# Kernel optimization log

Measured on AMD Instinct MI355X. Metric: run time of the kernel, lower is better.

## Reference

```python
import jax, jax.numpy as jnp
import numpy as np

DIM = 768
HEADS = 12
MLP_DIM = 3072
EPS = 1e-5


def setup_inputs() -> dict:
    key = jax.random.key(0)
    ks = jax.random.split(key, 10)
    s = lambda d: 1.0 / np.sqrt(d)
    return {
        "x": jax.random.normal(ks[0], (8, 1024, DIM), dtype=jnp.float32),
        "ln1_g": jnp.ones((DIM,), jnp.float32),
        "ln1_b": jnp.zeros((DIM,), jnp.float32),
        "w_qkv": jax.random.normal(ks[1], (DIM, 3 * DIM), jnp.float32) * s(DIM),
        "w_out": jax.random.normal(ks[2], (DIM, DIM), jnp.float32) * s(DIM),
        "b_out": jnp.zeros((DIM,), jnp.float32),
        "ln2_g": jnp.ones((DIM,), jnp.float32),
        "ln2_b": jnp.zeros((DIM,), jnp.float32),
        "w1": jax.random.normal(ks[3], (DIM, MLP_DIM), jnp.float32) * s(DIM),
        "b1": jnp.zeros((MLP_DIM,), jnp.float32),
        "w2": jax.random.normal(ks[4], (MLP_DIM, DIM), jnp.float32) * s(MLP_DIM),
        "b2": jnp.zeros((DIM,), jnp.float32),
    }


def _layernorm(x, g, b):
    mu = jnp.mean(x, axis=-1, keepdims=True)
    var = jnp.mean(jnp.square(x - mu), axis=-1, keepdims=True)
    return (x - mu) * jax.lax.rsqrt(var + EPS) * g + b


def _block(x, ln1_g, ln1_b, w_qkv, w_out, b_out, ln2_g, ln2_b, w1, b1, w2, b2):
    B, N, C = x.shape
    H = HEADS
    Dh = C // H
    scale = Dh ** -0.5
    # attention
    h = _layernorm(x, ln1_g, ln1_b)
    qkv = (h @ w_qkv).reshape(B, N, 3, H, Dh)
    q, k, v = qkv[:, :, 0], qkv[:, :, 1], qkv[:, :, 2]  # [B,N,H,Dh]
    attn = jnp.einsum("bnhd,bmhd->bhnm", q, k) * scale
    attn = jax.nn.softmax(attn, axis=-1)
    o = jnp.einsum("bhnm,bmhd->bnhd", attn, v).reshape(B, N, C)
    x = x + o @ w_out + b_out
    # mlp (exact erf GELU, matching torch nn.GELU default)
    h = _layernorm(x, ln2_g, ln2_b)
    h = jax.nn.gelu(h @ w1 + b1, approximate=False)
    x = x + h @ w2 + b2
    return x


def reference(x, ln1_g, ln1_b, w_qkv, w_out, b_out, ln2_g, ln2_b, w1, b1, w2, b2):
    return _block(x, ln1_g, ln1_b, w_qkv, w_out, b_out, ln2_g, ln2_b, w1, b1, w2, b2)
```

## Files before the change

### kernel.cpp

```cpp
#include <hip/hip_runtime.h>
#include <hip/hip_bf16.h>
#include <cstdint>

#define DIM 768
#define HEADS 12
#define DH 64
#define MLP_DIM 3072
#define ROWS 8192
#define SEQ 1024
#define PPAD 72

typedef __attribute__((ext_vector_type(8))) short bf16x8;
typedef __attribute__((ext_vector_type(4))) float f32x4;

typedef __attribute__((address_space(1))) void GV;
typedef __attribute__((address_space(3))) void SV;

__device__ inline void async16(const void* g, void* l) {
  __builtin_amdgcn_global_load_lds((GV*)(void*)g, (SV*)l, 16, 0, 0);
}

__device__ inline unsigned short f2b(float f) {
  union { float f; uint32_t u; } v; v.f = f;
  uint32_t u = v.u;
  return (unsigned short)((u + 0x7fffu + ((u >> 16) & 1u)) >> 16);
}

__device__ inline float gelu_f(float v) {
  float x = v * 0.70710678118654752f;
  float ax = fabsf(x);
  float t = 1.f / (1.f + 0.47047f * ax);
  float poly = t * (0.3480242f + t * (-0.0958798f + t * 0.7478556f));
  float erfv = 1.f - poly * __expf(-ax * ax);
  erfv = copysignf(erfv, x);
  return 0.5f * v * (1.f + erfv);
}

__global__ __launch_bounds__(256) void transpose_k(const float* __restrict__ in,
                                                   unsigned short* __restrict__ out,
                                                   int K, int N) {
  __shared__ float t[32][33];
  int tx = threadIdx.x & 31, ty = threadIdx.x >> 5;
  int bn = blockIdx.x * 32, bk = blockIdx.y * 32;
#pragma unroll
  for (int i = ty; i < 32; i += 8) t[i][tx] = in[(size_t)(bk + i) * N + bn + tx];
  __syncthreads();
#pragma unroll
  for (int i = ty; i < 32; i += 8) out[(size_t)(bn + i) * K + bk + tx] = f2b(t[tx][i]);
}

__global__ __launch_bounds__(256) void ln_k(const float* __restrict__ x,
                                            const float* __restrict__ g,
                                            const float* __restrict__ b,
                                            unsigned short* __restrict__ h) {
  int wave = threadIdx.x >> 6, lane = threadIdx.x & 63;
  int row = blockIdx.x * 4 + wave;
  const float* xr = x + (size_t)row * DIM;
  float v[12];
  float s = 0.f;
#pragma unroll
  for (int j = 0; j < 12; ++j) { v[j] = xr[lane + j * 64]; s += v[j]; }
#pragma unroll
  for (int m = 1; m < 64; m <<= 1) s += __shfl_xor(s, m);
  float mu = s * (1.f / DIM);
  float vs = 0.f;
#pragma unroll
  for (int j = 0; j < 12; ++j) { float d = v[j] - mu; vs += d * d; }
#pragma unroll
  for (int m = 1; m < 64; m <<= 1) vs += __shfl_xor(vs, m);
  float rstd = rsqrtf(vs * (1.f / DIM) + 1e-5f);
  unsigned short* hr = h + (size_t)row * DIM;
#pragma unroll
  for (int j = 0; j < 12; ++j) {
    int i = lane + j * 64;
    hr[i] = f2b((v[j] - mu) * rstd * g[i] + b[i]);
  }
}

template <int MODE, int TM>
__global__ __launch_bounds__(256, 2) void gemm_k(
    const unsigned short* __restrict__ A, const unsigned short* __restrict__ Bt,
    int M, int N, int K,
    const float* __restrict__ bias, const float* __restrict__ resid,
    float* __restrict__ outf, unsigned short* __restrict__ outb,
    unsigned short* __restrict__ Qb, unsigned short* __restrict__ Kb,
    unsigned short* __restrict__ Vt) {
  constexpr int MI = (TM == 128) ? 4 : 2;
  __shared__ __align__(16) unsigned short As[TM * 64];
  __shared__ __align__(16) unsigned short Bs[128 * 64];
  int tid = threadIdx.x;
  int wave = tid >> 6, lane = tid & 63, lrow = lane & 15, qd = lane >> 4;
  int ntn = N >> 7;
  int bm = (blockIdx.x / ntn) * TM;
  int bn = (blockIdx.x % ntn) << 7;
  int wm = (TM == 128) ? (wave >> 1) * 64 : (wave & 1) * 32;
  int wn = (TM == 128) ? (wave & 1) * 64 : (wave >> 1) * 64;

  f32x4 acc[MI][4];
#pragma unroll
  for (int i = 0; i < MI; ++i)
#pragma unroll
    for (int j = 0; j < 4; ++j) acc[i][j] = (f32x4){0.f, 0.f, 0.f, 0.f};

  int srow = tid >> 3;
  int c = (tid & 7) ^ (srow & 7);
  const char* gA = (const char*)(A + (size_t)(bm + srow) * K) + c * 16;
  const char* gB = (const char*)(Bt + (size_t)(bn + srow) * K) + c * 16;
  char* lA = (char*)As + tid * 16;
  char* lB = (char*)Bs + tid * 16;
  size_t rstep = (size_t)32 * K * 2;

  int nk = K >> 6;
  for (int kt = 0; kt < nk; ++kt) {
    size_t ko = (size_t)kt * 128;
#pragma unroll
    for (int j = 0; j < TM / 32; ++j) async16(gA + ko + j * rstep, lA + j * 4096);
#pragma unroll
    for (int j = 0; j < 4; ++j) async16(gB + ko + j * rstep, lB + j * 4096);
    asm volatile("s_waitcnt vmcnt(0)" ::: "memory");
    __syncthreads();
#pragma unroll
    for (int s = 0; s < 2; ++s) {
      int q = s * 4 + qd;
      bf16x8 af[MI], bfr[4];
#pragma unroll
      for (int i = 0; i < MI; ++i) {
        int r = wm + i * 16 + lrow;
        af[i] = *(const bf16x8*)(As + r * 64 + ((q ^ (r & 7)) << 3));
      }
#pragma unroll
      for (int i = 0; i < 4; ++i) {
        int r = wn + i * 16 + lrow;
        bfr[i] = *(const bf16x8*)(Bs + r * 64 + ((q ^ (r & 7)) << 3));
      }
#pragma unroll
      for (int mi = 0; mi < MI; ++mi)
#pragma unroll
        for (int ni = 0; ni < 4; ++ni)
          acc[mi][ni] = __builtin_amdgcn_mfma_f32_16x16x32_bf16(af[mi], bfr[ni], acc[mi][ni], 0, 0, 0);
    }
    __syncthreads();
  }

#pragma unroll
  for (int mi = 0; mi < MI; ++mi)
#pragma unroll
    for (int ni = 0; ni < 4; ++ni)
#pragma unroll
      for (int r = 0; r < 4; ++r) {
        int row = bm + wm + mi * 16 + qd * 4 + r;
        int col = bn + wn + ni * 16 + lrow;
        float v = acc[mi][ni][r];
        if (MODE == 0) {
          int which = col / 768;
          int rem = col - which * 768;
          int hh = rem >> 6, dh = rem & 63;
          int bb = row >> 10, n = row & 1023;
          size_t bh = (size_t)(bb * HEADS + hh);
          if (which == 0) {
            Qb[(bh * SEQ + n) * DH + dh] = f2b(v * 0.125f);
          } else if (which == 1) {
            Kb[(bh * SEQ + n) * DH + (((dh >> 3) ^ (n & 7)) << 3) + (dh & 7)] = f2b(v);
          } else {
            Vt[(bh * DH + dh) * SEQ + (n & ~63) +
               ((((n >> 3) & 7) ^ (dh & 7)) << 3) + (n & 7)] = f2b(v);
          }
        } else if (MODE == 1) {
          v += bias[col] + resid[(size_t)row * 768 + col];
          outf[(size_t)row * 768 + col] = v;
        } else {
          v += bias[col];
          outb[(size_t)row * MLP_DIM + col] = f2b(gelu_f(v));
        }
      }
}

__global__ __launch_bounds__(256, 3) void attn_k(const unsigned short* __restrict__ Qb,
                                                 const unsigned short* __restrict__ Kb,
                                                 const unsigned short* __restrict__ Vt,
                                                 unsigned short* __restrict__ o) {
  __shared__ __align__(16) unsigned short Ks[2][64 * 64];
  __shared__ __align__(16) unsigned short Vs[2][64 * 64];
  __shared__ __align__(16) unsigned short Pa[4][32 * PPAD];
  int tid = threadIdx.x;
  int wave = tid >> 6, lane = tid & 63;
  int lrow = lane & 15, qd = lane >> 4;
  int bh = blockIdx.x % 96;
  int qt = blockIdx.x / 96;
  int b = bh / HEADS, hh = bh % HEADS;
  const unsigned short* Qh = Qb + (size_t)bh * SEQ * DH;
  const char* Kh = (const char*)(Kb + (size_t)bh * SEQ * DH);
  const char* Vh = (const char*)(Vt + (size_t)bh * DH * SEQ);
  int qw = qt * 128 + wave * 32;

  bf16x8 qf[2][2];
#pragma unroll
  for (int qs = 0; qs < 2; ++qs)
#pragma unroll
    for (int hf = 0; hf < 2; ++hf)
      qf[qs][hf] = *(const bf16x8*)(Qh + (qw + qs * 16 + lrow) * DH + hf * 32 + qd * 8);

  f32x4 oacc[2][4];
#pragma unroll
  for (int qs = 0; qs < 2; ++qs)
#pragma unroll
    for (int d = 0; d < 4; ++d) oacc[qs][d] = (f32x4){0.f, 0.f, 0.f, 0.f};
  float li[2] = {0.f, 0.f};
  unsigned short* Pw = Pa[wave];

  auto stage = [&](int t, int buf) {
    const char* kbase = Kh + (size_t)t * 8192;
    char* kd = (char*)Ks[buf];
    async16(kbase + tid * 16, kd + tid * 16);
    async16(kbase + 4096 + tid * 16, kd + 4096 + tid * 16);
    const char* vbase = Vh + (size_t)t * 128;
    char* vd = (char*)Vs[buf];
    async16(vbase + (size_t)(tid >> 3) * 2048 + (tid & 7) * 16, vd + tid * 16);
    async16(vbase + (size_t)((tid >> 3) + 32) * 2048 + (tid & 7) * 16, vd + 4096 + tid * 16);
  };

  stage(0, 0);
  for (int t = 0; t < 16; ++t) {
    asm volatile("s_waitcnt vmcnt(0)" ::: "memory");
    __syncthreads();
    if (t < 15) stage(t + 1, (t + 1) & 1);
    const unsigned short* Kst = Ks[t & 1];
    const unsigned short* Vst = Vs[t & 1];

    f32x4 st[4][2];
#pragma unroll
    for (int kt = 0; kt < 4; ++kt) {
      int krow = kt * 16 + lrow;
      int ksw = krow & 7;
      const unsigned short* Kr = Kst + krow * 64;
      bf16x8 k0 = *(const bf16x8*)(Kr + ((qd ^ ksw) << 3));
      bf16x8 k1 = *(const bf16x8*)(Kr + (((qd + 4) ^ ksw) << 3));
#pragma unroll
      for (int qs = 0; qs < 2; ++qs) {
        f32x4 z = (f32x4){0.f, 0.f, 0.f, 0.f};
        z = __builtin_amdgcn_mfma_f32_16x16x32_bf16(k0, qf[qs][0], z, 0, 0, 0);
        z = __builtin_amdgcn_mfma_f32_16x16x32_bf16(k1, qf[qs][1], z, 0, 0, 0);
        st[kt][qs] = z;
      }
    }

#pragma unroll
    for (int kt = 0; kt < 4; ++kt)
#pragma unroll
      for (int qs = 0; qs < 2; ++qs) {
        float p0 = __expf(st[kt][qs][0]);
        float p1 = __expf(st[kt][qs][1]);
        float p2 = __expf(st[kt][qs][2]);
        float p3 = __expf(st[kt][qs][3]);
        li[qs] += (p0 + p1) + (p2 + p3);
        uint2 pk;
        pk.x = (uint32_t)f2b(p0) | ((uint32_t)f2b(p1) << 16);
        pk.y = (uint32_t)f2b(p2) | ((uint32_t)f2b(p3) << 16);
        *(uint2*)(Pw + (qs * 16 + lrow) * PPAD + kt * 16 + qd * 4) = pk;
      }
    asm volatile("s_waitcnt lgkmcnt(0)" ::: "memory");

    bf16x8 ap[2][2];
#pragma unroll
    for (int qs = 0; qs < 2; ++qs)
#pragma unroll
      for (int kh = 0; kh < 2; ++kh)
        ap[qs][kh] = *(const bf16x8*)(Pw + (qs * 16 + lrow) * PPAD + kh * 32 + qd * 8);

#pragma unroll
    for (int ds = 0; ds < 4; ++ds) {
      int vrow = ds * 16 + lrow;
      int vsw = vrow & 7;
      const unsigned short* Vr = Vst + vrow * 64;
      bf16x8 v0 = *(const bf16x8*)(Vr + ((qd ^ vsw) << 3));
      bf16x8 v1 = *(const bf16x8*)(Vr + (((4 + qd) ^ vsw) << 3));
#pragma unroll
      for (int qs = 0; qs < 2; ++qs) {
        oacc[qs][ds] = __builtin_amdgcn_mfma_f32_16x16x32_bf16(ap[qs][0], v0, oacc[qs][ds], 0, 0, 0);
        oacc[qs][ds] = __builtin_amdgcn_mfma_f32_16x16x32_bf16(ap[qs][1], v1, oacc[qs][ds], 0, 0, 0);
      }
    }
  }

#pragma unroll
  for (int qs = 0; qs < 2; ++qs) {
    li[qs] += __shfl_xor(li[qs], 16);
    li[qs] += __shfl_xor(li[qs], 32);
  }

#pragma unroll
  for (int qs = 0; qs < 2; ++qs)
#pragma unroll
    for (int r = 0; r < 4; ++r) {
      float inv = 1.f / __shfl(li[qs], qd * 4 + r);
      int n = qw + qs * 16 + qd * 4 + r;
#pragma unroll
      for (int ds = 0; ds < 4; ++ds) {
        int dh = ds * 16 + lrow;
        o[((size_t)(b * SEQ + n)) * DIM + hh * DH + dh] = f2b(oacc[qs][ds][r] * inv);
      }
    }
}

extern "C" void kernel_launch(void* const* d_in, const int* in_sizes, int n_in,
                              void* d_out, int out_size, void* d_ws, size_t ws_size,
                              hipStream_t stream) {
  const float* x     = (const float*)d_in[0];
  const float* ln1_g = (const float*)d_in[1];
  const float* ln1_b = (const float*)d_in[2];
  const float* w_qkv = (const float*)d_in[3];
  const float* w_out = (const float*)d_in[4];
  const float* b_out = (const float*)d_in[5];
  const float* ln2_g = (const float*)d_in[6];
  const float* ln2_b = (const float*)d_in[7];
  const float* w1    = (const float*)d_in[8];
  const float* b1    = (const float*)d_in[9];
  const float* w2    = (const float*)d_in[10];
  const float* b2    = (const float*)d_in[11];

  char* ws = (char*)d_ws;
  unsigned short* wqkvT = (unsigned short*)(ws + 0);
  unsigned short* woutT = (unsigned short*)(ws + 3538944);
  unsigned short* w1T   = (unsigned short*)(ws + 4718592);
  unsigned short* w2T   = (unsigned short*)(ws + 9437184);
  float*          x2    = (float*)(ws + 14155776);
  unsigned short* h     = (unsigned short*)(ws + 39321600);
  char* big = ws + 51904512;
  unsigned short* Qb = (unsigned short*)(big);
  unsigned short* Kb = (unsigned short*)(big + 12582912);
  unsigned short* Vt = (unsigned short*)(big + 25165824);
  unsigned short* ob = (unsigned short*)(big + 37748736);
  unsigned short* am = (unsigned short*)(big);

  transpose_k<<<dim3(72, 24), 256, 0, stream>>>(w_qkv, wqkvT, 768, 2304);
  transpose_k<<<dim3(24, 24), 256, 0, stream>>>(w_out, woutT, 768, 768);
  transpose_k<<<dim3(96, 24), 256, 0, stream>>>(w1, w1T, 768, 3072);
  transpose_k<<<dim3(24, 96), 256, 0, stream>>>(w2, w2T, 3072, 768);

  ln_k<<<2048, 256, 0, stream>>>(x, ln1_g, ln1_b, h);
  gemm_k<0, 128><<<64 * 18, 256, 0, stream>>>(h, wqkvT, ROWS, 2304, 768,
                                              nullptr, nullptr, nullptr, nullptr, Qb, Kb, Vt);
  attn_k<<<768, 256, 0, stream>>>(Qb, Kb, Vt, ob);
  gemm_k<1, 64><<<128 * 6, 256, 0, stream>>>(ob, woutT, ROWS, 768, 768,
                                             b_out, x, x2, nullptr, nullptr, nullptr, nullptr);
  ln_k<<<2048, 256, 0, stream>>>(x2, ln2_g, ln2_b, h);
  gemm_k<2, 128><<<64 * 24, 256, 0, stream>>>(h, w1T, ROWS, 3072, 768,
                                              b1, nullptr, nullptr, am, nullptr, nullptr, nullptr);
  gemm_k<1, 64><<<128 * 6, 256, 0, stream>>>(am, w2T, ROWS, 768, 3072,
                                             b2, x2, (float*)d_out, nullptr, nullptr, nullptr, nullptr);
}
```

Before: 357.1 us.

## Double-buffer GEMM K-loop and stage epilogue through LDS for coalesced stores

The GEMM main loop now uses two LDS buffers, so the async global-to-LDS load of the next K tile is issued while MFMAs run on the current tile, and one barrier per iteration is removed. The epilogue is also rewritten: each mode first writes the accumulator tile into shared memory, then issues 16-byte vector stores for Q/K/V (keeping the swizzled layouts), the residual-add output, and the GELU output, replacing scattered 2-byte and 4-byte stores. The cost is doubled LDS use per block, which may reduce occupancy, plus extra barriers and LDS traffic in the epilogue.

After: 391.4 us. +9.6%, slower.

```diff
diff --git a/kernel.cpp b/kernel.cpp
--- a/kernel.cpp
+++ b/kernel.cpp
@@ -9,6 +9,8 @@
 #define ROWS 8192
 #define SEQ 1024
 #define PPAD 72
+#define ISTR 136
+#define FSTR 132
 
 typedef __attribute__((ext_vector_type(8))) short bf16x8;
 typedef __attribute__((ext_vector_type(4))) float f32x4;
@@ -86,8 +88,8 @@
     unsigned short* __restrict__ Qb, unsigned short* __restrict__ Kb,
     unsigned short* __restrict__ Vt) {
   constexpr int MI = (TM == 128) ? 4 : 2;
-  __shared__ __align__(16) unsigned short As[TM * 64];
-  __shared__ __align__(16) unsigned short Bs[128 * 64];
+  constexpr int ASZ = TM * 64, BSZ = 128 * 64;
+  __shared__ __align__(16) unsigned short smem[2 * (ASZ + BSZ)];
   int tid = threadIdx.x;
   int wave = tid >> 6, lane = tid & 63, lrow = lane & 15, qd = lane >> 4;
   int ntn = N >> 7;
@@ -106,19 +108,26 @@
   int c = (tid & 7) ^ (srow & 7);
   const char* gA = (const char*)(A + (size_t)(bm + srow) * K) + c * 16;
   const char* gB = (const char*)(Bt + (size_t)(bn + srow) * K) + c * 16;
-  char* lA = (char*)As + tid * 16;
-  char* lB = (char*)Bs + tid * 16;
   size_t rstep = (size_t)32 * K * 2;
 
+  auto stage = [&](int kt, int buf) {
+    size_t ko = (size_t)kt * 128;
+    char* lA = (char*)(smem + (size_t)buf * (ASZ + BSZ)) + tid * 16;
+    char* lB = lA + ASZ * 2;
+#pragma unroll
+    for (int j = 0; j < TM / 32; ++j) async16(gA + ko + j * rstep, lA + j * 4096);
+#pragma unroll
+    for (int j = 0; j < 4; ++j) async16(gB + ko + j * rstep, lB + j * 4096);
+  };
+
   int nk = K >> 6;
+  stage(0, 0);
   for (int kt = 0; kt < nk; ++kt) {
-    size_t ko = (size_t)kt * 128;
-#pragma unroll
-    for (int j = 0; j < TM / 32; ++j) async16(gA + ko + j * rstep, lA + j * 4096);
-#pragma unroll
-    for (int j = 0; j < 4; ++j) async16(gB + ko + j * rstep, lB + j * 4096);
     asm volatile("s_waitcnt vmcnt(0)" ::: "memory");
     __syncthreads();
+    if (kt + 1 < nk) stage(kt + 1, (kt + 1) & 1);
+    const unsigned short* As = smem + (size_t)(kt & 1) * (ASZ + BSZ);
+    const unsigned short* Bs = As + ASZ;
 #pragma unroll
     for (int s = 0; s < 2; ++s) {
       int q = s * 4 + qd;
@@ -139,40 +148,108 @@
         for (int ni = 0; ni < 4; ++ni)
           acc[mi][ni] = __builtin_amdgcn_mfma_f32_16x16x32_bf16(af[mi], bfr[ni], acc[mi][ni], 0, 0, 0);
     }
+  }
+  __syncthreads();
+
+  if (MODE == 1) {
+    float* img = (float*)smem;
+#pragma unroll
+    for (int mi = 0; mi < MI; ++mi)
+#pragma unroll
+      for (int ni = 0; ni < 4; ++ni)
+#pragma unroll
+        for (int r = 0; r < 4; ++r)
+          img[(wm + mi * 16 + qd * 4 + r) * FSTR + wn + ni * 16 + lrow] = acc[mi][ni][r];
     __syncthreads();
+    int lr = tid >> 2, cs = (tid & 3) * 32;
+    const float* src = img + lr * FSTR + cs;
+    float* dst = outf + (size_t)(bm + lr) * 768 + bn + cs;
+    const float* bp = bias + bn + cs;
+    const float* rp = resid + (size_t)(bm + lr) * 768 + bn + cs;
+#pragma unroll
+    for (int k = 0; k < 8; ++k) {
+      f32x4 v = *(const f32x4*)(src + k * 4);
+      f32x4 bb = *(const f32x4*)(bp + k * 4);
+      f32x4 rr = *(const f32x4*)(rp + k * 4);
+      *(f32x4*)(dst + k * 4) = v + bb + rr;
+    }
+  } else if (MODE == 2) {
+    unsigned short* img = smem;
+#pragma unroll
+    for (int mi = 0; mi < MI; ++mi)
+#pragma unroll
+      for (int ni = 0; ni < 4; ++ni)
+#pragma unroll
+        for (int r = 0; r < 4; ++r) {
+          int lc = wn + ni * 16 + lrow;
+          float v = acc[mi][ni][r] + bias[bn + lc];
+          img[(wm + mi * 16 + qd * 4 + r) * ISTR + lc] = f2b(gelu_f(v));
+        }
+    __syncthreads();
+#pragma unroll
+    for (int p = 0; p < 2; ++p) {
+      int lr = p * 64 + (tid >> 2);
+      int cs = (tid & 3) * 32;
+      const unsigned short* src = img + lr * ISTR + cs;
+      unsigned short* dst = outb + (size_t)(bm + lr) * MLP_DIM + bn + cs;
+#pragma unroll
+      for (int k = 0; k < 4; ++k) *(uint4*)(dst + k * 8) = *(const uint4*)(src + k * 8);
+    }
+  } else {
+    int which = bn / 768;
+    int rem_base = bn - which * 768;
+    unsigned short* img = smem;
+    if (which < 2) {
+#pragma unroll
+      for (int mi = 0; mi < MI; ++mi)
+#pragma unroll
+        for (int ni = 0; ni < 4; ++ni)
+#pragma unroll
+          for (int r = 0; r < 4; ++r) {
+            float v = acc[mi][ni][r];
+            if (which == 0) v *= 0.125f;
+            img[(wm + mi * 16 + qd * 4 + r) * ISTR + wn + ni * 16 + lrow] = f2b(v);
+          }
+      __syncthreads();
+      int lr = tid >> 1, hseg = tid & 1;
+      int hh = rem_base / 64 + hseg;
+      int b = (bm + lr) >> 10, n = (bm + lr) & 1023;
+      size_t bh = (size_t)(b * HEADS + hh);
+      const unsigned short* src = img + lr * ISTR + hseg * 64;
+      unsigned short* dst = (which == 0 ? Qb : Kb) + (bh * SEQ + n) * DH;
+      if (which == 0) {
+#pragma unroll
+        for (int j = 0; j < 8; ++j) *(uint4*)(dst + j * 8) = *(const uint4*)(src + j * 8);
+      } else {
+        int nx = n & 7;
+#pragma unroll
+        for (int j = 0; j < 8; ++j) *(uint4*)(dst + ((j ^ nx) * 8)) = *(const uint4*)(src + j * 8);
+      }
+    } else {
+#pragma unroll
+      for (int mi = 0; mi < MI; ++mi)
+#pragma unroll
+        for (int ni = 0; ni < 4; ++ni) {
+          int lc = wn + ni * 16 + lrow;
+          int rbase = wm + mi * 16 + qd * 4;
+          uint2 pk;
+          pk.x = (uint32_t)f2b(acc[mi][ni][0]) | ((uint32_t)f2b(acc[mi][ni][1]) << 16);
+          pk.y = (uint32_t)f2b(acc[mi][ni][2]) | ((uint32_t)f2b(acc[mi][ni][3]) << 16);
+          *(uint2*)(img + lc * ISTR + rbase) = pk;
+        }
+      __syncthreads();
+      int d = tid >> 1, nh = tid & 1;
+      int hh = rem_base / 64 + (d >> 6);
+      int dhl = d & 63;
+      int b = bm >> 10;
+      size_t bh = (size_t)(b * HEADS + hh);
+      const unsigned short* src = img + d * ISTR + nh * 64;
+      unsigned short* dst = Vt + (bh * DH + dhl) * SEQ + (bm & 1023) + nh * 64;
+      int dx = dhl & 7;
+#pragma unroll
+      for (int j = 0; j < 8; ++j) *(uint4*)(dst + ((j ^ dx) * 8)) = *(const uint4*)(src + j * 8);
+    }
   }
-
-#pragma unroll
-  for (int mi = 0; mi < MI; ++mi)
-#pragma unroll
-    for (int ni = 0; ni < 4; ++ni)
-#pragma unroll
-      for (int r = 0; r < 4; ++r) {
-        int row = bm + wm + mi * 16 + qd * 4 + r;
-        int col = bn + wn + ni * 16 + lrow;
-        float v = acc[mi][ni][r];
-        if (MODE == 0) {
-          int which = col / 768;
-          int rem = col - which * 768;
-          int hh = rem >> 6, dh = rem & 63;
-          int bb = row >> 10, n = row & 1023;
-          size_t bh = (size_t)(bb * HEADS + hh);
-          if (which == 0) {
-            Qb[(bh * SEQ + n) * DH + dh] = f2b(v * 0.125f);
-          } else if (which == 1) {
-            Kb[(bh * SEQ + n) * DH + (((dh >> 3) ^ (n & 7)) << 3) + (dh & 7)] = f2b(v);
-          } else {
-            Vt[(bh * DH + dh) * SEQ + (n & ~63) +
-               ((((n >> 3) & 7) ^ (dh & 7)) << 3) + (n & 7)] = f2b(v);
-          }
-        } else if (MODE == 1) {
-          v += bias[col] + resid[(size_t)row * 768 + col];
-          outf[(size_t)row * 768 + col] = v;
-        } else {
-          v += bias[col];
-          outb[(size_t)row * MLP_DIM + col] = f2b(gelu_f(v));
-        }
-      }
 }
 
 __global__ __launch_bounds__(256, 3) void attn_k(const unsigned short* __restrict__ Qb,
```

## Register-prefetch next GEMM k-tile and stage GELU output through LDS

Applied to the files above, without the earlier changes.

Replaces the async global-to-LDS loads plus full vmcnt wait with register prefetch. The next k-tile is loaded into registers while MFMAs run on the current tile held in LDS. For the MLP-up GEMM, the bf16 GELU results are written to a padded LDS image and then stored to global memory as coalesced 16-byte vectors, instead of scattered 2-byte stores. This costs more registers, which at launch bounds of 2 may cause spills, and adds an extra barrier in the epilogue.

Result: no change. 363.3 us (+1.7%).

```diff
diff --git a/kernel.cpp b/kernel.cpp
--- a/kernel.cpp
+++ b/kernel.cpp
@@ -9,6 +9,7 @@
 #define ROWS 8192
 #define SEQ 1024
 #define PPAD 72
+#define ISTR 136
 
 typedef __attribute__((ext_vector_type(8))) short bf16x8;
 typedef __attribute__((ext_vector_type(4))) float f32x4;
@@ -80,14 +81,15 @@
 template <int MODE, int TM>
 __global__ __launch_bounds__(256, 2) void gemm_k(
     const unsigned short* __restrict__ A, const unsigned short* __restrict__ Bt,
-    int M, int N, int K,
+    int N, int K,
     const float* __restrict__ bias, const float* __restrict__ resid,
     float* __restrict__ outf, unsigned short* __restrict__ outb,
     unsigned short* __restrict__ Qb, unsigned short* __restrict__ Kb,
     unsigned short* __restrict__ Vt) {
   constexpr int MI = (TM == 128) ? 4 : 2;
-  __shared__ __align__(16) unsigned short As[TM * 64];
-  __shared__ __align__(16) unsigned short Bs[128 * 64];
+  constexpr int ASH = TM * 64;
+  constexpr int SMEMS = (TM == 128) ? ((MODE == 2) ? 128 * ISTR : 16384) : 12288;
+  __shared__ __align__(16) unsigned short smem[SMEMS];
   int tid = threadIdx.x;
   int wave = tid >> 6, lane = tid & 63, lrow = lane & 15, qd = lane >> 4;
   int ntn = N >> 7;
@@ -106,19 +108,51 @@
   int c = (tid & 7) ^ (srow & 7);
   const char* gA = (const char*)(A + (size_t)(bm + srow) * K) + c * 16;
   const char* gB = (const char*)(Bt + (size_t)(bn + srow) * K) + c * 16;
-  char* lA = (char*)As + tid * 16;
-  char* lB = (char*)Bs + tid * 16;
+  char* lA = (char*)smem + tid * 16;
+  char* lB = (char*)smem + ASH * 2 + tid * 16;
   size_t rstep = (size_t)32 * K * 2;
+
+  const unsigned short* As = smem;
+  const unsigned short* Bs = smem + ASH;
+
+  uint4 pa0, pa1, pa2, pa3, pb0, pb1, pb2, pb3;
+  pa0 = *(const uint4*)(gA);
+  pa1 = *(const uint4*)(gA + rstep);
+  if constexpr (TM == 128) {
+    pa2 = *(const uint4*)(gA + 2 * rstep);
+    pa3 = *(const uint4*)(gA + 3 * rstep);
+  }
+  pb0 = *(const uint4*)(gB);
+  pb1 = *(const uint4*)(gB + rstep);
+  pb2 = *(const uint4*)(gB + 2 * rstep);
+  pb3 = *(const uint4*)(gB + 3 * rstep);
 
   int nk = K >> 6;
   for (int kt = 0; kt < nk; ++kt) {
-    size_t ko = (size_t)kt * 128;
-#pragma unroll
-    for (int j = 0; j < TM / 32; ++j) async16(gA + ko + j * rstep, lA + j * 4096);
-#pragma unroll
-    for (int j = 0; j < 4; ++j) async16(gB + ko + j * rstep, lB + j * 4096);
-    asm volatile("s_waitcnt vmcnt(0)" ::: "memory");
+    *(uint4*)(lA) = pa0;
+    *(uint4*)(lA + 4096) = pa1;
+    if constexpr (TM == 128) {
+      *(uint4*)(lA + 8192) = pa2;
+      *(uint4*)(lA + 12288) = pa3;
+    }
+    *(uint4*)(lB) = pb0;
+    *(uint4*)(lB + 4096) = pb1;
+    *(uint4*)(lB + 8192) = pb2;
+    *(uint4*)(lB + 12288) = pb3;
     __syncthreads();
+    if (kt + 1 < nk) {
+      size_t k2 = (size_t)(kt + 1) * 128;
+      pa0 = *(const uint4*)(gA + k2);
+      pa1 = *(const uint4*)(gA + k2 + rstep);
+      if constexpr (TM == 128) {
+        pa2 = *(const uint4*)(gA + k2 + 2 * rstep);
+        pa3 = *(const uint4*)(gA + k2 + 3 * rstep);
+      }
+      pb0 = *(const uint4*)(gB + k2);
+      pb1 = *(const uint4*)(gB + k2 + rstep);
+      pb2 = *(const uint4*)(gB + k2 + 2 * rstep);
+      pb3 = *(const uint4*)(gB + k2 + 3 * rstep);
+    }
 #pragma unroll
     for (int s = 0; s < 2; ++s) {
       int q = s * 4 + qd;
@@ -142,16 +176,50 @@
     __syncthreads();
   }
 
-#pragma unroll
-  for (int mi = 0; mi < MI; ++mi)
-#pragma unroll
-    for (int ni = 0; ni < 4; ++ni)
-#pragma unroll
-      for (int r = 0; r < 4; ++r) {
-        int row = bm + wm + mi * 16 + qd * 4 + r;
-        int col = bn + wn + ni * 16 + lrow;
-        float v = acc[mi][ni][r];
-        if (MODE == 0) {
+  if (MODE == 1) {
+#pragma unroll
+    for (int mi = 0; mi < MI; ++mi)
+#pragma unroll
+      for (int ni = 0; ni < 4; ++ni)
+#pragma unroll
+        for (int r = 0; r < 4; ++r) {
+          int row = bm + wm + mi * 16 + qd * 4 + r;
+          int col = bn + wn + ni * 16 + lrow;
+          float v = acc[mi][ni][r] + bias[col] + resid[(size_t)row * 768 + col];
+          outf[(size_t)row * 768 + col] = v;
+        }
+  } else if (MODE == 2) {
+    unsigned short* img = smem;
+#pragma unroll
+    for (int mi = 0; mi < MI; ++mi)
+#pragma unroll
+      for (int ni = 0; ni < 4; ++ni)
+#pragma unroll
+        for (int r = 0; r < 4; ++r) {
+          int lc = wn + ni * 16 + lrow;
+          float v = acc[mi][ni][r] + bias[bn + lc];
+          img[(wm + mi * 16 + qd * 4 + r) * ISTR + lc] = f2b(gelu_f(v));
+        }
+    __syncthreads();
+#pragma unroll
+    for (int p = 0; p < 2; ++p) {
+      int lr = p * 64 + (tid >> 2);
+      int cs = (tid & 3) * 32;
+      const unsigned short* src = img + lr * ISTR + cs;
+      unsigned short* dst = outb + (size_t)(bm + lr) * MLP_DIM + bn + cs;
+#pragma unroll
+      for (int k = 0; k < 4; ++k) *(uint4*)(dst + k * 8) = *(const uint4*)(src + k * 8);
+    }
+  } else {
+#pragma unroll
+    for (int mi = 0; mi < MI; ++mi)
+#pragma unroll
+      for (int ni = 0; ni < 4; ++ni)
+#pragma unroll
+        for (int r = 0; r < 4; ++r) {
+          int row = bm + wm + mi * 16 + qd * 4 + r;
+          int col = bn + wn + ni * 16 + lrow;
+          float v = acc[mi][ni][r];
           int which = col / 768;
           int rem = col - which * 768;
           int hh = rem >> 6, dh = rem & 63;
@@ -165,14 +233,8 @@
             Vt[(bh * DH + dh) * SEQ + (n & ~63) +
                ((((n >> 3) & 7) ^ (dh & 7)) << 3) + (n & 7)] = f2b(v);
           }
-        } else if (MODE == 1) {
-          v += bias[col] + resid[(size_t)row * 768 + col];
-          outf[(size_t)row * 768 + col] = v;
-        } else {
-          v += bias[col];
-          outb[(size_t)row * MLP_DIM + col] = f2b(gelu_f(v));
         }
-      }
+  }
 }
 
 __global__ __launch_bounds__(256, 3) void attn_k(const unsigned short* __restrict__ Qb,
@@ -338,14 +400,14 @@
   transpose_k<<<dim3(24, 96), 256, 0, stream>>>(w2, w2T, 3072, 768);
 
   ln_k<<<2048, 256, 0, stream>>>(x, ln1_g, ln1_b, h);
-  gemm_k<0, 128><<<64 * 18, 256, 0, stream>>>(h, wqkvT, ROWS, 2304, 768,
+  gemm_k<0, 128><<<64 * 18, 256, 0, stream>>>(h, wqkvT, 2304, 768,
                                               nullptr, nullptr, nullptr, nullptr, Qb, Kb, Vt);
   attn_k<<<768, 256, 0, stream>>>(Qb, Kb, Vt, ob);
-  gemm_k<1, 64><<<128 * 6, 256, 0, stream>>>(ob, woutT, ROWS, 768, 768,
+  gemm_k<1, 64><<<128 * 6, 256, 0, stream>>>(ob, woutT, 768, 768,
                                              b_out, x, x2, nullptr, nullptr, nullptr, nullptr);
   ln_k<<<2048, 256, 0, stream>>>(x2, ln2_g, ln2_b, h);
-  gemm_k<2, 128><<<64 * 24, 256, 0, stream>>>(h, w1T, ROWS, 3072, 768,
+  gemm_k<2, 128><<<64 * 24, 256, 0, stream>>>(h, w1T, 3072, 768,
                                               b1, nullptr, nullptr, am, nullptr, nullptr, nullptr);
-  gemm_k<1, 64><<<128 * 6, 256, 0, stream>>>(am, w2T, ROWS, 768, 3072,
+  gemm_k<1, 64><<<128 * 6, 256, 0, stream>>>(am, w2T, 768, 3072,
                                              b2, x2, (float*)d_out, nullptr, nullptr, nullptr, nullptr);
 }
```
